# Kernel optimization log

Measured on AMD Instinct MI355X. Metric: run time of the kernel, lower is better.

## Reference

```python
import jax, jax.numpy as jnp
import numpy as np

N_NODES = 50000
N_EDGES = 800000
DIM = 128
HEADS = 4
NEG_SLOPE = 0.2
LN_EPS = 1e-5


def setup_inputs() -> dict:
    key = jax.random.key(0)
    ks = jax.random.split(key, 8)
    x = jax.random.normal(ks[0], (N_NODES, DIM), dtype=jnp.float32)
    edge_index = jax.random.randint(ks[1], (2, N_EDGES), 0, N_NODES, dtype=jnp.int32)
    W = jax.random.normal(ks[2], (DIM, DIM), dtype=jnp.float32) * (1.0 / np.sqrt(DIM))
    b = jnp.zeros((DIM,), dtype=jnp.float32)
    C = DIM // HEADS
    att_src = jax.random.normal(ks[3], (HEADS, C), dtype=jnp.float32) * 0.1
    att_dst = jax.random.normal(ks[4], (HEADS, C), dtype=jnp.float32) * 0.1
    ln_gamma = jnp.ones((DIM,), dtype=jnp.float32)
    ln_beta = jnp.zeros((DIM,), dtype=jnp.float32)
    prelu_w = jnp.full((1,), 0.25, dtype=jnp.float32)
    return {"x": x, "edge_index": edge_index, "W": W, "b": b,
            "att_src": att_src, "att_dst": att_dst,
            "ln_gamma": ln_gamma, "ln_beta": ln_beta, "prelu_w": prelu_w}


def reference(x, edge_index, W, b, att_src, att_dst, ln_gamma, ln_beta, prelu_w):
    N, D = x.shape
    H = HEADS
    C = D // H
    # shared linear transform (PyG GATConv lin_src == lin_dst for homogeneous input)
    xw = (x @ W).reshape(N, H, C)                      # [N,H,C]
    a_src = jnp.einsum('nhc,hc->nh', xw, att_src)      # [N,H]
    a_dst = jnp.einsum('nhc,hc->nh', xw, att_dst)      # [N,H]
    # add self loops (PyG default add_self_loops=True)
    loop = jnp.arange(N, dtype=edge_index.dtype)
    src = jnp.concatenate([edge_index[0], loop])       # [E+N]
    dst = jnp.concatenate([edge_index[1], loop])       # [E+N]
    # per-edge attention logits + segment softmax over destination
    alpha = jax.nn.leaky_relu(a_src[src] + a_dst[dst], NEG_SLOPE)   # [E+N,H]
    amax = jax.ops.segment_max(alpha, dst, num_segments=N)          # [N,H]
    alpha = jnp.exp(alpha - amax[dst])
    denom = jax.ops.segment_sum(alpha, dst, num_segments=N)         # [N,H]
    alpha = alpha / denom[dst]
    # weighted aggregation of source features
    msg = xw[src] * alpha[:, :, None]                               # [E+N,H,C]
    out = jax.ops.segment_sum(msg, dst, num_segments=N).reshape(N, D) + b
    # residual + LayerNorm + PReLU
    h = x + out
    mu = jnp.mean(h, axis=-1, keepdims=True)
    var = jnp.mean(jnp.square(h - mu), axis=-1, keepdims=True)
    h = (h - mu) * jax.lax.rsqrt(var + LN_EPS) * ln_gamma + ln_beta
    return jnp.where(h > 0, h, prelu_w[0] * h)
```

## Files before the change

kernel.cpp:

```cpp
#include <hip/hip_runtime.h>

#define NNODES 50000
#define NEDGES 800000
#define NEDGE4 200000
#define DIMF 128
#define NHEADS 4
#define NEG_SLOPE 0.2f
#define LN_EPS 1e-5f
#define SLOTS 64
#define NPERX 6250
#define CSRBLK 1024

__device__ __forceinline__ unsigned short f2bf(float f) {
    unsigned int u = __float_as_uint(f);
    u = (u + 0x7fffu + ((u >> 16) & 1u)) >> 16;
    return (unsigned short)u;
}

__global__ __launch_bounds__(256) void k_linear(
    const float* __restrict__ x, const float* __restrict__ W,
    const float* __restrict__ att_src, const float* __restrict__ att_dst,
    unsigned short* __restrict__ xwb,
    float* __restrict__ asrc, float* __restrict__ adst,
    int* __restrict__ cursor)
{
    __shared__ float4 Ws4[32 * 32];
    __shared__ float  xs[64][132];
    const int tid = threadIdx.x;
    const int r8  = tid >> 5;
    const int c32 = tid & 31;
    const int base = blockIdx.x * 64;

    if (tid < 64 && base + tid < NNODES) cursor[base + tid] = 0;

    {
        const float4* x4 = (const float4*)x;
        #pragma unroll
        for (int j = 0; j < 8; ++j) {
            int idx = tid + j * 256;
            int r = idx >> 5, q = idx & 31;
            int gr = base + r;
            float4 v = make_float4(0.f, 0.f, 0.f, 0.f);
            if (gr < NNODES) v = x4[(size_t)gr * 32 + q];
            ((float4*)(&xs[r][0]))[q] = v;
        }
    }

    float accf[8][4];
    #pragma unroll
    for (int i = 0; i < 8; ++i)
        #pragma unroll
        for (int j = 0; j < 4; ++j) accf[i][j] = 0.f;

    const float4* W4 = (const float4*)W;
    for (int qt = 0; qt < 4; ++qt) {
        __syncthreads();
        #pragma unroll
        for (int j = 0; j < 4; ++j)
            Ws4[tid + j * 256] = W4[qt * 1024 + tid + j * 256];
        __syncthreads();
        for (int k4 = 0; k4 < 32; k4 += 4) {
            float xv[8][4];
            #pragma unroll
            for (int i = 0; i < 8; ++i)
                *(float4*)&xv[i][0] = *(const float4*)&xs[i * 8 + r8][qt * 32 + k4];
            #pragma unroll
            for (int kk = 0; kk < 4; ++kk) {
                float4 w4 = Ws4[((k4 + kk) << 5) | c32];
                #pragma unroll
                for (int i = 0; i < 8; ++i) {
                    accf[i][0] += xv[i][kk] * w4.x;
                    accf[i][1] += xv[i][kk] * w4.y;
                    accf[i][2] += xv[i][kk] * w4.z;
                    accf[i][3] += xv[i][kk] * w4.w;
                }
            }
        }
    }

    const int head = c32 >> 3;
    const float* As = att_src + head * 32 + (c32 & 7) * 4;
    const float* Ad = att_dst + head * 32 + (c32 & 7) * 4;
    float a0 = As[0], a1 = As[1], a2 = As[2], a3 = As[3];
    float d0 = Ad[0], d1 = Ad[1], d2 = Ad[2], d3 = Ad[3];
    ushort4* xwb4 = (ushort4*)xwb;

    #pragma unroll
    for (int i = 0; i < 8; ++i) {
        const int row = i * 8 + r8;
        const int grow = base + row;
        float ps = accf[i][0] * a0 + accf[i][1] * a1 + accf[i][2] * a2 + accf[i][3] * a3;
        float pd = accf[i][0] * d0 + accf[i][1] * d1 + accf[i][2] * d2 + accf[i][3] * d3;
        #pragma unroll
        for (int o = 1; o < 8; o <<= 1) {
            ps += __shfl_xor(ps, o);
            pd += __shfl_xor(pd, o);
        }
        if (grow < NNODES) {
            ushort4 u;
            u.x = f2bf(accf[i][0]); u.y = f2bf(accf[i][1]);
            u.z = f2bf(accf[i][2]); u.w = f2bf(accf[i][3]);
            xwb4[(size_t)grow * 32 + c32] = u;
            if ((tid & 7) == 0) {
                asrc[grow * NHEADS + head] = ps;
                adst[grow * NHEADS + head] = pd;
            }
        }
    }
}

__global__ __launch_bounds__(256) void k_scatter(
    const int* __restrict__ esrc, const int* __restrict__ edst,
    const float4* __restrict__ asrc4, const float4* __restrict__ adst4,
    int* __restrict__ cursor, unsigned short* __restrict__ perm,
    ushort4* __restrict__ wperm)
{
    const int lo = (blockIdx.x & 7) * NPERX, hi = lo + NPERX;
    const int stride = (CSRBLK >> 3) * 256;
    const int4* es4 = (const int4*)esrc;
    const int4* ed4 = (const int4*)edst;
    for (int e = (blockIdx.x >> 3) * 256 + threadIdx.x; e < NEDGE4; e += stride) {
        int4 d4 = ed4[e];
        int4 s4 = es4[e];
        #define DO_EDGE(DD, SS)                                               \
        if (DD >= lo && DD < hi) {                                            \
            int p = atomicAdd(&cursor[DD], 1);                                \
            if (p < SLOTS) {                                                  \
                perm[(size_t)DD * SLOTS + p] = (unsigned short)(SS);          \
                float4 av = asrc4[SS];                                        \
                float4 dv = adst4[DD];                                        \
                float l0 = av.x + dv.x, l1 = av.y + dv.y;                     \
                float l2 = av.z + dv.z, l3 = av.w + dv.w;                     \
                l0 = (l0 > 0.f) ? l0 : NEG_SLOPE * l0;                        \
                l1 = (l1 > 0.f) ? l1 : NEG_SLOPE * l1;                        \
                l2 = (l2 > 0.f) ? l2 : NEG_SLOPE * l2;                        \
                l3 = (l3 > 0.f) ? l3 : NEG_SLOPE * l3;                        \
                ushort4 wu;                                                   \
                wu.x = f2bf(__expf(l0)); wu.y = f2bf(__expf(l1));             \
                wu.z = f2bf(__expf(l2)); wu.w = f2bf(__expf(l3));             \
                wperm[(size_t)DD * SLOTS + p] = wu;                          \
            }                                                                 \
        }
        DO_EDGE(d4.x, s4.x)
        DO_EDGE(d4.y, s4.y)
        DO_EDGE(d4.z, s4.z)
        DO_EDGE(d4.w, s4.w)
        #undef DO_EDGE
    }
}

__global__ __launch_bounds__(256) void k_gat(
    const float* __restrict__ x, const float* __restrict__ bias,
    const float* __restrict__ asrc, const float* __restrict__ adst,
    const unsigned int* __restrict__ xwb,
    const int* __restrict__ cursor, const unsigned short* __restrict__ perm,
    const unsigned short* __restrict__ wperm_u16,
    const float* __restrict__ ln_g, const float* __restrict__ ln_b,
    const float* __restrict__ prelu_w, float* __restrict__ out)
{
    const int wid  = (blockIdx.x * 256 + threadIdx.x) >> 6;
    const int lane = threadIdx.x & 63;
    if (wid >= NNODES) return;
    const int myh = lane >> 4;
    const int hb  = lane & 3;

    const float adh_b = adst[wid * NHEADS + hb];
    float lgS = asrc[wid * NHEADS + hb] + adh_b;
    lgS = (lgS > 0.f) ? lgS : NEG_SLOPE * lgS;
    const float wself_b = __expf(lgS);

    int cnt = cursor[wid];
    if (cnt > SLOTS) cnt = SLOTS;
    int sidx = (lane < cnt) ? (int)perm[(size_t)wid * SLOTS + lane] : 0;

    const float wself = __shfl(wself_b, myh);
    const unsigned int vself = xwb[(size_t)wid * 64 + lane];
    float acc0 = wself * __uint_as_float(vself << 16);
    float acc1 = wself * __uint_as_float(vself & 0xffff0000u);
    float dsum = 0.f;

    const int jmax = (cnt + 15) >> 4;
    for (int j = 0; j < jmax; ++j) {
        const unsigned short wu = wperm_u16[(size_t)wid * 256 + j * 64 + lane];
        const int eslot = j * 16 + (lane >> 2);
        const float wv = (eslot < cnt) ? __uint_as_float(((unsigned)wu) << 16) : 0.f;
        dsum += wv;

        #pragma unroll
        for (int b = 0; b < 2; ++b) {
            const int ebase = j * 16 + b * 8;
            int s_[8]; float w_[8]; unsigned v_[8];
            #pragma unroll
            for (int e = 0; e < 8; ++e) {
                s_[e] = __shfl(sidx, ebase + e);
                w_[e] = __shfl(wv, ((b * 8 + e) << 2) | myh);
            }
            #pragma unroll
            for (int e = 0; e < 8; ++e)
                v_[e] = xwb[(size_t)s_[e] * 64 + lane];
            #pragma unroll
            for (int e = 0; e < 8; ++e) {
                acc0 += w_[e] * __uint_as_float(v_[e] << 16);
                acc1 += w_[e] * __uint_as_float(v_[e] & 0xffff0000u);
            }
        }
    }

    #pragma unroll
    for (int o = 4; o < 64; o <<= 1) dsum += __shfl_xor(dsum, o);
    const float wsum = __shfl(dsum + wself_b, myh);

    const float inv = 1.0f / wsum;
    const int c = lane * 2;
    const float2 xr = ((const float2*)x)[(size_t)wid * 64 + lane];
    float h0 = xr.x + acc0 * inv + bias[c];
    float h1 = xr.y + acc1 * inv + bias[c + 1];

    float s1 = h0 + h1, s2 = h0 * h0 + h1 * h1;
    #pragma unroll
    for (int o = 1; o < 64; o <<= 1) {
        s1 += __shfl_xor(s1, o);
        s2 += __shfl_xor(s2, o);
    }
    const float mu  = s1 * (1.f / 128.f);
    const float var = s2 * (1.f / 128.f) - mu * mu;
    const float r   = rsqrtf(var + LN_EPS);

    float g0 = (h0 - mu) * r * ln_g[c]     + ln_b[c];
    float g1 = (h1 - mu) * r * ln_g[c + 1] + ln_b[c + 1];
    const float pw = prelu_w[0];
    g0 = (g0 > 0.f) ? g0 : pw * g0;
    g1 = (g1 > 0.f) ? g1 : pw * g1;

    ((float2*)out)[(size_t)wid * 64 + lane] = make_float2(g0, g1);
}

extern "C" void kernel_launch(void* const* d_in, const int* in_sizes, int n_in,
                              void* d_out, int out_size, void* d_ws, size_t ws_size,
                              hipStream_t stream)
{
    const float* x    = (const float*)d_in[0];
    const int*   eidx = (const int*)  d_in[1];
    const float* W    = (const float*)d_in[2];
    const float* bias = (const float*)d_in[3];
    const float* attS = (const float*)d_in[4];
    const float* attD = (const float*)d_in[5];
    const float* lng  = (const float*)d_in[6];
    const float* lnb  = (const float*)d_in[7];
    const float* pre  = (const float*)d_in[8];

    const int* esrc = eidx;
    const int* edst = eidx + NEDGES;

    unsigned short* xwb = (unsigned short*)d_ws;
    float* asrc    = (float*)(xwb + (size_t)NNODES * DIMF);
    float* adst    = asrc + (size_t)NNODES * NHEADS;
    int*   cursor  = (int*)(adst + (size_t)NNODES * NHEADS);
    unsigned short* perm = (unsigned short*)(cursor + NNODES);
    ushort4* wperm = (ushort4*)(perm + (size_t)NNODES * SLOTS);

    k_linear<<<dim3((NNODES + 63) / 64), dim3(256), 0, stream>>>(
        x, W, attS, attD, xwb, asrc, adst, cursor);

    k_scatter<<<dim3(CSRBLK), dim3(256), 0, stream>>>(
        esrc, edst, (const float4*)asrc, (const float4*)adst,
        cursor, perm, wperm);

    k_gat<<<dim3((NNODES * 64 + 255) / 256), dim3(256), 0, stream>>>(
        x, bias, asrc, adst, (const unsigned int*)xwb, cursor, perm,
        (const unsigned short*)wperm, lng, lnb, pre, (float*)d_out);
}
```

Before: 123.4 us.

## Move edge attention weight computation from scatter into aggregation kernel

```diff
diff --git a/kernel.cpp b/kernel.cpp
--- a/kernel.cpp
+++ b/kernel.cpp
@@ -9,7 +9,10 @@
 #define LN_EPS 1e-5f
 #define SLOTS 64
 #define NPERX 6250
-#define CSRBLK 1024
+#define CSRBLK 2048
+
+typedef int   v4i __attribute__((ext_vector_type(4)));
+typedef float v2f __attribute__((ext_vector_type(2)));
 
 __device__ __forceinline__ unsigned short f2bf(float f) {
     unsigned int u = __float_as_uint(f);
@@ -111,50 +114,31 @@
 
 __global__ __launch_bounds__(256) void k_scatter(
     const int* __restrict__ esrc, const int* __restrict__ edst,
-    const float4* __restrict__ asrc4, const float4* __restrict__ adst4,
-    int* __restrict__ cursor, unsigned short* __restrict__ perm,
-    ushort4* __restrict__ wperm)
+    int* __restrict__ cursor, unsigned short* __restrict__ perm)
 {
     const int lo = (blockIdx.x & 7) * NPERX, hi = lo + NPERX;
     const int stride = (CSRBLK >> 3) * 256;
-    const int4* es4 = (const int4*)esrc;
-    const int4* ed4 = (const int4*)edst;
+    const v4i* es4 = (const v4i*)esrc;
+    const v4i* ed4 = (const v4i*)edst;
     for (int e = (blockIdx.x >> 3) * 256 + threadIdx.x; e < NEDGE4; e += stride) {
-        int4 d4 = ed4[e];
-        int4 s4 = es4[e];
-        #define DO_EDGE(DD, SS)                                               \
-        if (DD >= lo && DD < hi) {                                            \
-            int p = atomicAdd(&cursor[DD], 1);                                \
-            if (p < SLOTS) {                                                  \
-                perm[(size_t)DD * SLOTS + p] = (unsigned short)(SS);          \
-                float4 av = asrc4[SS];                                        \
-                float4 dv = adst4[DD];                                        \
-                float l0 = av.x + dv.x, l1 = av.y + dv.y;                     \
-                float l2 = av.z + dv.z, l3 = av.w + dv.w;                     \
-                l0 = (l0 > 0.f) ? l0 : NEG_SLOPE * l0;                        \
-                l1 = (l1 > 0.f) ? l1 : NEG_SLOPE * l1;                        \
-                l2 = (l2 > 0.f) ? l2 : NEG_SLOPE * l2;                        \
-                l3 = (l3 > 0.f) ? l3 : NEG_SLOPE * l3;                        \
-                ushort4 wu;                                                   \
-                wu.x = f2bf(__expf(l0)); wu.y = f2bf(__expf(l1));             \
-                wu.z = f2bf(__expf(l2)); wu.w = f2bf(__expf(l3));             \
-                wperm[(size_t)DD * SLOTS + p] = wu;                          \
-            }                                                                 \
-        }
-        DO_EDGE(d4.x, s4.x)
-        DO_EDGE(d4.y, s4.y)
-        DO_EDGE(d4.z, s4.z)
-        DO_EDGE(d4.w, s4.w)
-        #undef DO_EDGE
+        v4i d4 = __builtin_nontemporal_load(ed4 + e);
+        v4i s4 = __builtin_nontemporal_load(es4 + e);
+        #pragma unroll
+        for (int c = 0; c < 4; ++c) {
+            const int dd = d4[c], ss = s4[c];
+            if (dd >= lo && dd < hi) {
+                int p = atomicAdd(&cursor[dd], 1);
+                if (p < SLOTS) perm[(size_t)dd * SLOTS + p] = (unsigned short)ss;
+            }
+        }
     }
 }
 
 __global__ __launch_bounds__(256) void k_gat(
     const float* __restrict__ x, const float* __restrict__ bias,
-    const float* __restrict__ asrc, const float* __restrict__ adst,
+    const float4* __restrict__ asrc4, const float4* __restrict__ adst4,
     const unsigned int* __restrict__ xwb,
     const int* __restrict__ cursor, const unsigned short* __restrict__ perm,
-    const unsigned short* __restrict__ wperm_u16,
     const float* __restrict__ ln_g, const float* __restrict__ ln_b,
     const float* __restrict__ prelu_w, float* __restrict__ out)
 {
@@ -162,53 +146,77 @@
     const int lane = threadIdx.x & 63;
     if (wid >= NNODES) return;
     const int myh = lane >> 4;
-    const int hb  = lane & 3;
-
-    const float adh_b = adst[wid * NHEADS + hb];
-    float lgS = asrc[wid * NHEADS + hb] + adh_b;
-    lgS = (lgS > 0.f) ? lgS : NEG_SLOPE * lgS;
-    const float wself_b = __expf(lgS);
 
     int cnt = cursor[wid];
     if (cnt > SLOTS) cnt = SLOTS;
-    int sidx = (lane < cnt) ? (int)perm[(size_t)wid * SLOTS + lane] : 0;
-
-    const float wself = __shfl(wself_b, myh);
+    const int sidx = (lane < cnt) ? (int)perm[(size_t)wid * SLOTS + lane] : 0;
+
+    const float4 dvw = adst4[wid];
+    const float4 avw = asrc4[wid];
+
+    const float4 ae = asrc4[sidx];
+    float e0 = ae.x + dvw.x, e1 = ae.y + dvw.y;
+    float e2 = ae.z + dvw.z, e3 = ae.w + dvw.w;
+    e0 = (e0 > 0.f) ? e0 : NEG_SLOPE * e0;
+    e1 = (e1 > 0.f) ? e1 : NEG_SLOPE * e1;
+    e2 = (e2 > 0.f) ? e2 : NEG_SLOPE * e2;
+    e3 = (e3 > 0.f) ? e3 : NEG_SLOPE * e3;
+    const bool act = (lane < cnt);
+    const float w0 = act ? __expf(e0) : 0.f;
+    const float w1 = act ? __expf(e1) : 0.f;
+    const float w2 = act ? __expf(e2) : 0.f;
+    const float w3 = act ? __expf(e3) : 0.f;
+    const unsigned wy = (unsigned)f2bf(w0) | ((unsigned)f2bf(w1) << 16);
+    const unsigned wz = (unsigned)f2bf(w2) | ((unsigned)f2bf(w3) << 16);
+
+    float r0 = __uint_as_float(wy << 16);
+    float r1 = __uint_as_float(wy & 0xffff0000u);
+    float r2 = __uint_as_float(wz << 16);
+    float r3 = __uint_as_float(wz & 0xffff0000u);
+    #pragma unroll
+    for (int o = 1; o < 64; o <<= 1) {
+        r0 += __shfl_xor(r0, o);
+        r1 += __shfl_xor(r1, o);
+        r2 += __shfl_xor(r2, o);
+        r3 += __shfl_xor(r3, o);
+    }
+
+    const float av_h = (myh == 0) ? avw.x : (myh == 1) ? avw.y : (myh == 2) ? avw.z : avw.w;
+    const float dv_h = (myh == 0) ? dvw.x : (myh == 1) ? dvw.y : (myh == 2) ? dvw.z : dvw.w;
+    float lgS = av_h + dv_h;
+    lgS = (lgS > 0.f) ? lgS : NEG_SLOPE * lgS;
+    const float wself = __expf(lgS);
+    const float dsel = (myh == 0) ? r0 : (myh == 1) ? r1 : (myh == 2) ? r2 : r3;
+    const float wsum = dsel + wself;
+
     const unsigned int vself = xwb[(size_t)wid * 64 + lane];
     float acc0 = wself * __uint_as_float(vself << 16);
     float acc1 = wself * __uint_as_float(vself & 0xffff0000u);
-    float dsum = 0.f;
-
-    const int jmax = (cnt + 15) >> 4;
-    for (int j = 0; j < jmax; ++j) {
-        const unsigned short wu = wperm_u16[(size_t)wid * 256 + j * 64 + lane];
-        const int eslot = j * 16 + (lane >> 2);
-        const float wv = (eslot < cnt) ? __uint_as_float(((unsigned)wu) << 16) : 0.f;
-        dsum += wv;
-
+
+    for (int j = 0; j * 16 < cnt; ++j) {
         #pragma unroll
         for (int b = 0; b < 2; ++b) {
             const int ebase = j * 16 + b * 8;
-            int s_[8]; float w_[8]; unsigned v_[8];
+            int s_[8]; unsigned wy_[8], wz_[8], v_[8];
             #pragma unroll
             for (int e = 0; e < 8; ++e) {
-                s_[e] = __shfl(sidx, ebase + e);
-                w_[e] = __shfl(wv, ((b * 8 + e) << 2) | myh);
+                s_[e]  = __shfl(sidx, ebase + e);
+                wy_[e] = (unsigned)__shfl((int)wy, ebase + e);
+                wz_[e] = (unsigned)__shfl((int)wz, ebase + e);
             }
             #pragma unroll
             for (int e = 0; e < 8; ++e)
                 v_[e] = xwb[(size_t)s_[e] * 64 + lane];
             #pragma unroll
             for (int e = 0; e < 8; ++e) {
-                acc0 += w_[e] * __uint_as_float(v_[e] << 16);
-                acc1 += w_[e] * __uint_as_float(v_[e] & 0xffff0000u);
-            }
-        }
-    }
-
-    #pragma unroll
-    for (int o = 4; o < 64; o <<= 1) dsum += __shfl_xor(dsum, o);
-    const float wsum = __shfl(dsum + wself_b, myh);
+                const unsigned wp = (myh < 2) ? wy_[e] : wz_[e];
+                const float w = __uint_as_float((myh & 1) ? (wp & 0xffff0000u)
+                                                          : (wp << 16));
+                acc0 += w * __uint_as_float(v_[e] << 16);
+                acc1 += w * __uint_as_float(v_[e] & 0xffff0000u);
+            }
+        }
+    }
 
     const float inv = 1.0f / wsum;
     const int c = lane * 2;
@@ -232,7 +240,8 @@
     g0 = (g0 > 0.f) ? g0 : pw * g0;
     g1 = (g1 > 0.f) ? g1 : pw * g1;
 
-    ((float2*)out)[(size_t)wid * 64 + lane] = make_float2(g0, g1);
+    v2f gv; gv.x = g0; gv.y = g1;
+    __builtin_nontemporal_store(gv, (v2f*)out + (size_t)wid * 64 + lane);
 }
 
 extern "C" void kernel_launch(void* const* d_in, const int* in_sizes, int n_in,
@@ -257,16 +266,13 @@
     float* adst    = asrc + (size_t)NNODES * NHEADS;
     int*   cursor  = (int*)(adst + (size_t)NNODES * NHEADS);
     unsigned short* perm = (unsigned short*)(cursor + NNODES);
-    ushort4* wperm = (ushort4*)(perm + (size_t)NNODES * SLOTS);
 
     k_linear<<<dim3((NNODES + 63) / 64), dim3(256), 0, stream>>>(
         x, W, attS, attD, xwb, asrc, adst, cursor);
 
-    k_scatter<<<dim3(CSRBLK), dim3(256), 0, stream>>>(
-        esrc, edst, (const float4*)asrc, (const float4*)adst,
-        cursor, perm, wperm);
+    k_scatter<<<dim3(CSRBLK), dim3(256), 0, stream>>>(esrc, edst, cursor, perm);
 
     k_gat<<<dim3((NNODES * 64 + 255) / 256), dim3(256), 0, stream>>>(
-        x, bias, asrc, adst, (const unsigned int*)xwb, cursor, perm,
-        (const unsigned short*)wperm, lng, lnb, pre, (float*)d_out);
-}
+        x, bias, (const float4*)asrc, (const float4*)adst,
+        (const unsigned int*)xwb, cursor, perm, lng, lnb, pre, (float*)d_out);
+}
```

Result: slower. 138.3 us (+12.1%).

## Split edge weight computation out of atomic scatter into per-node kernel

Applied to the files above, without the earlier changes.

```diff
diff --git a/kernel.cpp b/kernel.cpp
--- a/kernel.cpp
+++ b/kernel.cpp
@@ -9,7 +9,10 @@
 #define LN_EPS 1e-5f
 #define SLOTS 64
 #define NPERX 6250
-#define CSRBLK 1024
+#define CSRBLK 2048
+
+typedef int   v4i __attribute__((ext_vector_type(4)));
+typedef float v2f __attribute__((ext_vector_type(2)));
 
 __device__ __forceinline__ unsigned short f2bf(float f) {
     unsigned int u = __float_as_uint(f);
@@ -111,42 +114,53 @@
 
 __global__ __launch_bounds__(256) void k_scatter(
     const int* __restrict__ esrc, const int* __restrict__ edst,
-    const float4* __restrict__ asrc4, const float4* __restrict__ adst4,
-    int* __restrict__ cursor, unsigned short* __restrict__ perm,
-    ushort4* __restrict__ wperm)
+    int* __restrict__ cursor, unsigned short* __restrict__ perm)
 {
     const int lo = (blockIdx.x & 7) * NPERX, hi = lo + NPERX;
     const int stride = (CSRBLK >> 3) * 256;
-    const int4* es4 = (const int4*)esrc;
-    const int4* ed4 = (const int4*)edst;
+    const v4i* es4 = (const v4i*)esrc;
+    const v4i* ed4 = (const v4i*)edst;
     for (int e = (blockIdx.x >> 3) * 256 + threadIdx.x; e < NEDGE4; e += stride) {
-        int4 d4 = ed4[e];
-        int4 s4 = es4[e];
-        #define DO_EDGE(DD, SS)                                               \
-        if (DD >= lo && DD < hi) {                                            \
-            int p = atomicAdd(&cursor[DD], 1);                                \
-            if (p < SLOTS) {                                                  \
-                perm[(size_t)DD * SLOTS + p] = (unsigned short)(SS);          \
-                float4 av = asrc4[SS];                                        \
-                float4 dv = adst4[DD];                                        \
-                float l0 = av.x + dv.x, l1 = av.y + dv.y;                     \
-                float l2 = av.z + dv.z, l3 = av.w + dv.w;                     \
-                l0 = (l0 > 0.f) ? l0 : NEG_SLOPE * l0;                        \
-                l1 = (l1 > 0.f) ? l1 : NEG_SLOPE * l1;                        \
-                l2 = (l2 > 0.f) ? l2 : NEG_SLOPE * l2;                        \
-                l3 = (l3 > 0.f) ? l3 : NEG_SLOPE * l3;                        \
-                ushort4 wu;                                                   \
-                wu.x = f2bf(__expf(l0)); wu.y = f2bf(__expf(l1));             \
-                wu.z = f2bf(__expf(l2)); wu.w = f2bf(__expf(l3));             \
-                wperm[(size_t)DD * SLOTS + p] = wu;                          \
-            }                                                                 \
-        }
-        DO_EDGE(d4.x, s4.x)
-        DO_EDGE(d4.y, s4.y)
-        DO_EDGE(d4.z, s4.z)
-        DO_EDGE(d4.w, s4.w)
-        #undef DO_EDGE
-    }
+        v4i d4 = __builtin_nontemporal_load(ed4 + e);
+        v4i s4 = __builtin_nontemporal_load(es4 + e);
+        #pragma unroll
+        for (int c = 0; c < 4; ++c) {
+            const int dd = d4[c], ss = s4[c];
+            if (dd >= lo && dd < hi) {
+                int p = atomicAdd(&cursor[dd], 1);
+                if (p < SLOTS) perm[(size_t)dd * SLOTS + p] = (unsigned short)ss;
+            }
+        }
+    }
+}
+
+__global__ __launch_bounds__(256) void k_weights(
+    const float4* __restrict__ asrc4, const float4* __restrict__ adst4,
+    const int* __restrict__ cursor, const unsigned short* __restrict__ perm,
+    ushort4* __restrict__ wperm)
+{
+    const int wid  = (blockIdx.x * 256 + threadIdx.x) >> 6;
+    const int lane = threadIdx.x & 63;
+    if (wid >= NNODES) return;
+
+    int cnt = cursor[wid];
+    if (cnt > SLOTS) cnt = SLOTS;
+    const float4 dv = adst4[wid];
+
+    ushort4 wu = make_ushort4(0, 0, 0, 0);
+    if (lane < cnt) {
+        const int s = (int)perm[(size_t)wid * SLOTS + lane];
+        const float4 ae = asrc4[s];
+        float l0 = ae.x + dv.x, l1 = ae.y + dv.y;
+        float l2 = ae.z + dv.z, l3 = ae.w + dv.w;
+        l0 = (l0 > 0.f) ? l0 : NEG_SLOPE * l0;
+        l1 = (l1 > 0.f) ? l1 : NEG_SLOPE * l1;
+        l2 = (l2 > 0.f) ? l2 : NEG_SLOPE * l2;
+        l3 = (l3 > 0.f) ? l3 : NEG_SLOPE * l3;
+        wu.x = f2bf(__expf(l0)); wu.y = f2bf(__expf(l1));
+        wu.z = f2bf(__expf(l2)); wu.w = f2bf(__expf(l3));
+    }
+    wperm[(size_t)wid * SLOTS + lane] = wu;
 }
 
 __global__ __launch_bounds__(256) void k_gat(
@@ -171,7 +185,7 @@
 
     int cnt = cursor[wid];
     if (cnt > SLOTS) cnt = SLOTS;
-    int sidx = (lane < cnt) ? (int)perm[(size_t)wid * SLOTS + lane] : 0;
+    const int sidx = (lane < cnt) ? (int)perm[(size_t)wid * SLOTS + lane] : 0;
 
     const float wself = __shfl(wself_b, myh);
     const unsigned int vself = xwb[(size_t)wid * 64 + lane];
@@ -182,8 +196,7 @@
     const int jmax = (cnt + 15) >> 4;
     for (int j = 0; j < jmax; ++j) {
         const unsigned short wu = wperm_u16[(size_t)wid * 256 + j * 64 + lane];
-        const int eslot = j * 16 + (lane >> 2);
-        const float wv = (eslot < cnt) ? __uint_as_float(((unsigned)wu) << 16) : 0.f;
+        const float wv = __uint_as_float(((unsigned)wu) << 16);
         dsum += wv;
 
         #pragma unroll
@@ -232,7 +245,8 @@
     g0 = (g0 > 0.f) ? g0 : pw * g0;
     g1 = (g1 > 0.f) ? g1 : pw * g1;
 
-    ((float2*)out)[(size_t)wid * 64 + lane] = make_float2(g0, g1);
+    v2f gv; gv.x = g0; gv.y = g1;
+    __builtin_nontemporal_store(gv, (v2f*)out + (size_t)wid * 64 + lane);
 }
 
 extern "C" void kernel_launch(void* const* d_in, const int* in_sizes, int n_in,
@@ -262,9 +276,10 @@
     k_linear<<<dim3((NNODES + 63) / 64), dim3(256), 0, stream>>>(
         x, W, attS, attD, xwb, asrc, adst, cursor);
 
-    k_scatter<<<dim3(CSRBLK), dim3(256), 0, stream>>>(
-        esrc, edst, (const float4*)asrc, (const float4*)adst,
-        cursor, perm, wperm);
+    k_scatter<<<dim3(CSRBLK), dim3(256), 0, stream>>>(esrc, edst, cursor, perm);
+
+    k_weights<<<dim3((NNODES * 64 + 255) / 256), dim3(256), 0, stream>>>(
+        (const float4*)asrc, (const float4*)adst, cursor, perm, wperm);
 
     k_gat<<<dim3((NNODES * 64 + 255) / 256), dim3(256), 0, stream>>>(
         x, bias, asrc, adst, (const unsigned int*)xwb, cursor, perm,
```

New measurement: 132.9 us. 7.7% more time.
